# Kernel tuning notes

Hardware: AMD Instinct MI355X
Metric: run time of the kernel (lower is better)

## Reference

```python
import jax, jax.numpy as jnp
import numpy as np
from math import sqrt

B, T, I, H, O, R = 128, 1000, 3, 512, 1, 2
NOISE_STD = 0.05
ALPHA = 0.2


def setup_inputs() -> dict:
    key = jax.random.key(0)
    ks = jax.random.split(key, 6)
    inp = jax.random.normal(ks[0], (B, T, I), dtype=jnp.float32)
    noise = jax.random.normal(ks[1], (B, T, H), dtype=jnp.float32)
    # parameters initialized as in the torch module
    wi = jax.random.normal(ks[2], (I, H), dtype=jnp.float32)
    si = jnp.ones((I,), dtype=jnp.float32)
    m = jax.random.normal(ks[3], (H, R), dtype=jnp.float32) * (1.0 / sqrt(H))
    n = jax.random.normal(ks[4], (H, R), dtype=jnp.float32) * (1.0 / sqrt(H))
    wo = jax.random.normal(ks[5], (H, O), dtype=jnp.float32) * (2.0 / H)
    so = jnp.ones((O,), dtype=jnp.float32)
    h0 = jnp.zeros((H,), dtype=jnp.float32)
    return {"input": inp, "noise": noise, "wi": wi, "si": si, "m": m,
            "n": n, "wo": wo, "so": so, "h0": h0}


def reference(input, noise, wi, si, m, n, wo, so, h0):
    # proxy parameters: wi_full = (wi.T * si).T, wo_full = wo * so
    wi_full = si[:, None] * wi          # (I, H)
    wo_full = wo * so                   # (H, O)
    batch = input.shape[0]
    h_init = jnp.broadcast_to(h0, (batch, h0.shape[0]))  # (B, H)

    def step(h, xs):
        x_t, z_t = xs                   # (B, I), (B, H)
        r = jnp.tanh(h)
        rec = (r @ n) @ m.T             # low-rank recurrence, (B, H)
        h_new = h + NOISE_STD * z_t + ALPHA * (-h + rec + x_t @ wi_full)
        out = jnp.tanh(h_new) @ wo_full  # (B, O)
        return h_new, (out, h_new)

    xs = (jnp.swapaxes(input, 0, 1), jnp.swapaxes(noise, 0, 1))  # time-major
    _, (outs, hs) = jax.lax.scan(step, h_init, xs)
    output = jnp.swapaxes(outs, 0, 1)               # (B, T, O)
    trajectories = jnp.concatenate(
        [h_init[:, None, :], jnp.swapaxes(hs, 0, 1)], axis=1)  # (B, T+1, H)
    return output, trajectories
```

## Files before the change

kernel.cpp:

```cpp
#include <hip/hip_runtime.h>
#include <stdint.h>

#define B_ 128
#define T_ 1000
#define H_ 512
#define PH 8
#define NPHASE 125

typedef float vfloat4 __attribute__((ext_vector_type(4)));
typedef float vfloat2 __attribute__((ext_vector_type(2)));

template <int CTRL>
__device__ __forceinline__ float dpp_add(float x) {
    int moved = __builtin_amdgcn_update_dpp(0, __float_as_int(x), CTRL, 0xf, 0xf, true);
    return x + __int_as_float(moved);
}

__device__ __forceinline__ void wave_reduce2(float& p0, float& p1) {
    p0 = dpp_add<0x111>(p0); p1 = dpp_add<0x111>(p1);
    p0 = dpp_add<0x112>(p0); p1 = dpp_add<0x112>(p1);
    p0 = dpp_add<0x114>(p0); p1 = dpp_add<0x114>(p1);
    p0 = dpp_add<0x118>(p0); p1 = dpp_add<0x118>(p1);
    p0 = dpp_add<0x142>(p0); p1 = dpp_add<0x142>(p1);
    p0 = dpp_add<0x143>(p0); p1 = dpp_add<0x143>(p1);
}

__device__ __forceinline__ float wave_reduce1(float p) {
    p = dpp_add<0x111>(p); p = dpp_add<0x112>(p); p = dpp_add<0x114>(p);
    p = dpp_add<0x118>(p); p = dpp_add<0x142>(p); p = dpp_add<0x143>(p);
    return p;
}

__device__ __forceinline__ float fast_tanh(float x) {
    float E = __builtin_amdgcn_exp2f(x * 2.885390081777927f);
    float r = __builtin_amdgcn_rcpf(E + 1.0f);
    return __builtin_fmaf(-2.0f, r, 1.0f);
}

#define C2_ 2.885390081777927f

__device__ __forceinline__ vfloat2 bc2(float x) { vfloat2 v = {x, x}; return v; }

__global__ __launch_bounds__(128, 1) void lowrank_rnn_kernel(
    const float* __restrict__ input,
    const float* __restrict__ noise,
    const float* __restrict__ wi,
    const float* __restrict__ si,
    const float* __restrict__ m,
    const float* __restrict__ n,
    const float* __restrict__ wo,
    const float* __restrict__ so,
    const float* __restrict__ h0,
    float* __restrict__ out)
{
    const int b    = blockIdx.x;
    const int tid  = threadIdx.x;
    const int wid  = tid >> 6;
    const int lane = tid & 63;
    const int j0   = lane * 8;

    __shared__ __align__(16) vfloat4 ub[2][PH][2][64];
    __shared__ __align__(16) vfloat4 rb[2][PH][2][64];
    __shared__ __align__(16) vfloat4 hb[2][PH][2][64];
    __shared__ __align__(16) vfloat4 rfin[2][64];
    __shared__ __align__(16) vfloat4 hfin[2][64];
    __shared__ float os[T_ + 1];
    __shared__ int   flags[2];

    if (tid == 0) { flags[0] = 0; flags[1] = 0; }
    __syncthreads();
    volatile int* vprod = &flags[0];
    volatile int* vcons = &flags[1];

    if (wid == 1) {
        float wS0[8], wS1[8], wS2[8], wof[8];
        {
            const float so0 = so[0];
            #pragma unroll
            for (int i = 0; i < 3; ++i) {
                float s = 0.2f * si[i];
                float* dst = (i == 0) ? wS0 : (i == 1) ? wS1 : wS2;
                #pragma unroll
                for (int q = 0; q < 2; ++q) {
                    vfloat4 vw = *(const vfloat4*)(wi + i * H_ + j0 + 4 * q);
                    dst[4*q] = vw.x * s; dst[4*q+1] = vw.y * s;
                    dst[4*q+2] = vw.z * s; dst[4*q+3] = vw.w * s;
                }
            }
            #pragma unroll
            for (int q = 0; q < 2; ++q) {
                vfloat4 vw = *(const vfloat4*)(wo + j0 + 4 * q);
                wof[4*q] = vw.x * so0; wof[4*q+1] = vw.y * so0;
                wof[4*q+2] = vw.z * so0; wof[4*q+3] = vw.w * so0;
            }
        }
        const float* zb = noise + (size_t)b * T_ * H_ + j0;
        const float* xb = input + (size_t)b * T_ * 3;
        float* trajBase = out + (size_t)B_ * T_ + (size_t)b * (T_ + 1) * H_;

        {
            vfloat4 a = *(const vfloat4*)(h0 + j0);
            vfloat4 c = *(const vfloat4*)(h0 + j0 + 4);
            *(vfloat4*)(trajBase + j0)     = a;
            *(vfloat4*)(trajBase + j0 + 4) = c;
        }

        auto emit_phase = [&](int pp) {
            const int hf = pp & 1;
            #pragma unroll
            for (int s = 0; s < PH; ++s) {
                const int t = pp * PH + s;
                vfloat4 rl = rb[hf][s][0][lane];
                vfloat4 rh = rb[hf][s][1][lane];
                float p2 = rl.x * wof[0];
                p2 = __builtin_fmaf(rl.y, wof[1], p2);
                p2 = __builtin_fmaf(rl.z, wof[2], p2);
                p2 = __builtin_fmaf(rl.w, wof[3], p2);
                p2 = __builtin_fmaf(rh.x, wof[4], p2);
                p2 = __builtin_fmaf(rh.y, wof[5], p2);
                p2 = __builtin_fmaf(rh.z, wof[6], p2);
                p2 = __builtin_fmaf(rh.w, wof[7], p2);
                p2 = wave_reduce1(p2);
                if (lane == 63) os[t] = p2;
                vfloat4 hl = hb[hf][s][0][lane];
                vfloat4 hh = hb[hf][s][1][lane];
                float* tr = trajBase + (size_t)t * H_ + j0;
                *(vfloat4*)tr       = hl;
                *(vfloat4*)(tr + 4) = hh;
            }
        };

        for (int q = 0; q < NPHASE; ++q) {
            if (q >= 2) {
                while (*vcons < q - 1) {}
                asm volatile("" ::: "memory");
            }
            vfloat4 zl[PH], zh[PH];
            #pragma unroll
            for (int s = 0; s < PH; ++s) {
                const float* g = zb + (size_t)(q * PH + s) * H_;
                zl[s] = *(const vfloat4*)g;
                zh[s] = *(const vfloat4*)(g + 4);
            }
            if (q >= 2) emit_phase(q - 2);
            const int half = q & 1;
            #pragma unroll
            for (int s = 0; s < PH; ++s) {
                const int t = q * PH + s;
                float x0 = xb[3*t], x1 = xb[3*t+1], x2 = xb[3*t+2];
                float zz[8] = {zl[s].x, zl[s].y, zl[s].z, zl[s].w,
                               zh[s].x, zh[s].y, zh[s].z, zh[s].w};
                float u[8];
                #pragma unroll
                for (int k = 0; k < 8; ++k) {
                    float xw = __builtin_fmaf(x0, wS0[k],
                               __builtin_fmaf(x1, wS1[k], x2 * wS2[k]));
                    u[k] = __builtin_fmaf(zz[k], 0.05f, xw);
                }
                vfloat4 ulo = {u[0], u[1], u[2], u[3]};
                vfloat4 uhi = {u[4], u[5], u[6], u[7]};
                ub[half][s][0][lane] = ulo;
                ub[half][s][1][lane] = uhi;
            }
            asm volatile("s_waitcnt lgkmcnt(0)" ::: "memory");
            if (lane == 0) *vprod = q + 1;
        }
        while (*vcons < NPHASE) {}
        asm volatile("" ::: "memory");
        emit_phase(NPHASE - 2);
        emit_phase(NPHASE - 1);
        while (*vcons < NPHASE + 1) {}
        asm volatile("" ::: "memory");
        {
            vfloat4 rl = rfin[0][lane], rh = rfin[1][lane];
            float p2 = rl.x * wof[0];
            p2 = __builtin_fmaf(rl.y, wof[1], p2);
            p2 = __builtin_fmaf(rl.z, wof[2], p2);
            p2 = __builtin_fmaf(rl.w, wof[3], p2);
            p2 = __builtin_fmaf(rh.x, wof[4], p2);
            p2 = __builtin_fmaf(rh.y, wof[5], p2);
            p2 = __builtin_fmaf(rh.z, wof[6], p2);
            p2 = __builtin_fmaf(rh.w, wof[7], p2);
            p2 = wave_reduce1(p2);
            if (lane == 63) os[T_] = p2;
            float* tr = trajBase + (size_t)T_ * H_ + j0;
            *(vfloat4*)tr       = hfin[0][lane];
            *(vfloat4*)(tr + 4) = hfin[1][lane];
        }
        asm volatile("s_waitcnt lgkmcnt(0)" ::: "memory");
        float* outp = out + (size_t)b * T_;
        for (int idx = lane; idx < T_; idx += 64)
            outp[idx] = os[idx + 1];
    } else {
        vfloat2 n02[4], n12[4], m02[4], m12[4];
        vfloat2 bP[2][4], Tc[2][4], Dc[2][4];
        {
            const float* nb = n + 2 * j0;
            const float* mb = m + 2 * j0;
            #pragma unroll
            for (int q = 0; q < 4; ++q) {
                vfloat4 vn = *(const vfloat4*)(nb + 4 * q);
                vfloat2 a = {vn.x, vn.z}; n02[q] = a;
                vfloat2 c = {vn.y, vn.w}; n12[q] = c;
                vfloat4 vm = *(const vfloat4*)(mb + 4 * q);
                vfloat2 d = {0.2f * vm.x, 0.2f * vm.z}; m02[q] = d;
                vfloat2 e = {0.2f * vm.y, 0.2f * vm.w}; m12[q] = e;
            }
            #pragma unroll
            for (int q = 0; q < 2; ++q) {
                vfloat4 vh = *(const vfloat4*)(h0 + j0 + 4 * q);
                vfloat2 lo = {vh.x, vh.y}, hi = {vh.z, vh.w};
                bP[0][2*q] = lo; bP[0][2*q+1] = hi;
            }
            #pragma unroll
            for (int j = 0; j < 4; ++j) {
                vfloat2 T = {fast_tanh(bP[0][j].x), fast_tanh(bP[0][j].y)};
                Tc[0][j] = T;
                Dc[0][j] = 1.0f - T * T;
            }
        }
        float a0s = 0.0f, a1s = 0.0f;

        for (int p = 0; p < NPHASE; ++p) {
            while (*vprod < p + 1) {}
            asm volatile("" ::: "memory");
            const int half = p & 1;
            vfloat4 cul = ub[half][0][0][lane];
            vfloat4 cuh = ub[half][0][1][lane];
            #pragma unroll
            for (int s = 0; s < PH; ++s) {
                const int pp = s & 1;
                const int np = pp ^ 1;
                vfloat4 nul, nuh;
                if (s < PH - 1) {
                    nul = ub[half][s+1][0][lane];
                    nuh = ub[half][s+1][1][lane];
                }
                vfloat2 a02 = bc2(a0s), a12 = bc2(a1s);

                vfloat2 dl[4], r2[4], h2[4];
                #pragma unroll
                for (int j = 0; j < 4; ++j)
                    dl[j] = a02 * m02[j] + a12 * m12[j];
                #pragma unroll
                for (int j = 0; j < 4; ++j) {
                    vfloat2 t1 = Tc[pp][j] * dl[j];
                    vfloat2 e  = dl[j] - t1 * dl[j];
                    r2[j] = Dc[pp][j] * e + Tc[pp][j];
                }
                vfloat2 A0 = r2[1] * n02[1] + r2[0] * n02[0];
                vfloat2 B0 = r2[3] * n02[3] + r2[2] * n02[2];
                vfloat2 P0 = A0 + B0;
                float p0 = P0.x + P0.y;
                vfloat2 A1 = r2[1] * n12[1] + r2[0] * n12[0];
                vfloat2 B1 = r2[3] * n12[3] + r2[2] * n12[2];
                vfloat2 P1 = A1 + B1;
                float p1 = P1.x + P1.y;
                wave_reduce2(p0, p1);

                vfloat2 u2[4];
                vfloat2 t0 = {cul.x, cul.y}; u2[0] = t0;
                vfloat2 t1v = {cul.z, cul.w}; u2[1] = t1v;
                vfloat2 t2 = {cuh.x, cuh.y}; u2[2] = t2;
                vfloat2 t3 = {cuh.z, cuh.w}; u2[3] = t3;
                #pragma unroll
                for (int j = 0; j < 4; ++j) {
                    h2[j] = bP[pp][j] + dl[j];
                    bP[np][j] = h2[j] * 0.8f + u2[j];
                }
                #pragma unroll
                for (int j = 0; j < 4; ++j) {
                    vfloat2 x2 = bP[np][j] * C2_;
                    vfloat2 E  = {__builtin_amdgcn_exp2f(x2.x),
                                  __builtin_amdgcn_exp2f(x2.y)};
                    vfloat2 DD = E + 1.0f;
                    vfloat2 R  = {__builtin_amdgcn_rcpf(DD.x),
                                  __builtin_amdgcn_rcpf(DD.y)};
                    vfloat2 T  = bc2(-2.0f) * R + 1.0f;
                    Tc[np][j] = T;
                    Dc[np][j] = 1.0f - T * T;
                }

                vfloat4 rlo = {r2[0].x, r2[0].y, r2[1].x, r2[1].y};
                vfloat4 rhi = {r2[2].x, r2[2].y, r2[3].x, r2[3].y};
                rb[half][s][0][lane] = rlo;
                rb[half][s][1][lane] = rhi;
                vfloat4 hlo = {h2[0].x, h2[0].y, h2[1].x, h2[1].y};
                vfloat4 hhi = {h2[2].x, h2[2].y, h2[3].x, h2[3].y};
                hb[half][s][0][lane] = hlo;
                hb[half][s][1][lane] = hhi;

                a0s = __int_as_float(__builtin_amdgcn_readlane(__float_as_int(p0), 63));
                a1s = __int_as_float(__builtin_amdgcn_readlane(__float_as_int(p1), 63));

                cul = nul; cuh = nuh;
            }
            asm volatile("s_waitcnt lgkmcnt(0)" ::: "memory");
            if (lane == 0) *vcons = p + 1;
        }
        while (*vprod < NPHASE) {}
        asm volatile("" ::: "memory");
        vfloat2 a02 = bc2(a0s), a12 = bc2(a1s);
        float r[8], hT8[8];
        #pragma unroll
        for (int j = 0; j < 4; ++j) {
            vfloat2 dlt = a02 * m02[j] + a12 * m12[j];
            vfloat2 hT  = bP[0][j] + dlt;
            hT8[2*j] = hT.x; hT8[2*j+1] = hT.y;
            r[2*j]   = fast_tanh(hT.x);
            r[2*j+1] = fast_tanh(hT.y);
        }
        vfloat4 rlo = {r[0], r[1], r[2], r[3]};
        vfloat4 rhi = {r[4], r[5], r[6], r[7]};
        rfin[0][lane] = rlo;
        rfin[1][lane] = rhi;
        vfloat4 hlo = {hT8[0], hT8[1], hT8[2], hT8[3]};
        vfloat4 hhi = {hT8[4], hT8[5], hT8[6], hT8[7]};
        hfin[0][lane] = hlo;
        hfin[1][lane] = hhi;
        asm volatile("s_waitcnt lgkmcnt(0)" ::: "memory");
        if (lane == 0) *vcons = NPHASE + 1;
    }
}

extern "C" void kernel_launch(void* const* d_in, const int* in_sizes, int n_in,
                              void* d_out, int out_size, void* d_ws, size_t ws_size,
                              hipStream_t stream) {
    const float* input = (const float*)d_in[0];
    const float* noise = (const float*)d_in[1];
    const float* wi    = (const float*)d_in[2];
    const float* si    = (const float*)d_in[3];
    const float* m     = (const float*)d_in[4];
    const float* n     = (const float*)d_in[5];
    const float* wo    = (const float*)d_in[6];
    const float* so    = (const float*)d_in[7];
    const float* h0    = (const float*)d_in[8];
    float* out = (float*)d_out;

    hipLaunchKernelGGL(lowrank_rnn_kernel, dim3(B_), dim3(128), 0, stream,
                       input, noise, wi, si, m, n, wo, so, h0, out);
}
```

Before: 294.5 us.

## Double phase length and recompute tanh in producer wave instead of LDS r buffer

Raises the steps per synchronisation phase from 8 to 16, so there are half as many producer/consumer flag handshakes, and adds a tail phase of 8 steps for the remainder. The recurrence wave no longer writes tanh(h) to LDS. The helper wave recomputes tanh from the stored h when forming the output projection, which takes LDS stores off the critical serial path. In exchange the helper wave does extra transcendental work per step, and noise loads are split into two half-phase batches to limit register pressure.

```diff
diff --git a/kernel.cpp b/kernel.cpp
--- a/kernel.cpp
+++ b/kernel.cpp
@@ -4,8 +4,8 @@
 #define B_ 128
 #define T_ 1000
 #define H_ 512
-#define PH 8
-#define NPHASE 125
+#define PH 16
+#define NFULL 62
 
 typedef float vfloat4 __attribute__((ext_vector_type(4)));
 typedef float vfloat2 __attribute__((ext_vector_type(2)));
@@ -60,9 +60,7 @@
     const int j0   = lane * 8;
 
     __shared__ __align__(16) vfloat4 ub[2][PH][2][64];
-    __shared__ __align__(16) vfloat4 rb[2][PH][2][64];
     __shared__ __align__(16) vfloat4 hb[2][PH][2][64];
-    __shared__ __align__(16) vfloat4 rfin[2][64];
     __shared__ __align__(16) vfloat4 hfin[2][64];
     __shared__ float os[T_ + 1];
     __shared__ int   flags[2];
@@ -105,51 +103,41 @@
             *(vfloat4*)(trajBase + j0 + 4) = c;
         }
 
-        auto emit_phase = [&](int pp) {
+        auto emit_half = [&](int pp, int hh) {
             const int hf = pp & 1;
             #pragma unroll
-            for (int s = 0; s < PH; ++s) {
+            for (int s8 = 0; s8 < 8; ++s8) {
+                const int s = hh * 8 + s8;
                 const int t = pp * PH + s;
-                vfloat4 rl = rb[hf][s][0][lane];
-                vfloat4 rh = rb[hf][s][1][lane];
-                float p2 = rl.x * wof[0];
-                p2 = __builtin_fmaf(rl.y, wof[1], p2);
-                p2 = __builtin_fmaf(rl.z, wof[2], p2);
-                p2 = __builtin_fmaf(rl.w, wof[3], p2);
-                p2 = __builtin_fmaf(rh.x, wof[4], p2);
-                p2 = __builtin_fmaf(rh.y, wof[5], p2);
-                p2 = __builtin_fmaf(rh.z, wof[6], p2);
-                p2 = __builtin_fmaf(rh.w, wof[7], p2);
+                vfloat4 hl = hb[hf][s][0][lane];
+                vfloat4 hh4 = hb[hf][s][1][lane];
+                float r0 = fast_tanh(hl.x), r1 = fast_tanh(hl.y);
+                float r2 = fast_tanh(hl.z), r3 = fast_tanh(hl.w);
+                float r4 = fast_tanh(hh4.x), r5 = fast_tanh(hh4.y);
+                float r6 = fast_tanh(hh4.z), r7 = fast_tanh(hh4.w);
+                float p2 = r0 * wof[0];
+                p2 = __builtin_fmaf(r1, wof[1], p2);
+                p2 = __builtin_fmaf(r2, wof[2], p2);
+                p2 = __builtin_fmaf(r3, wof[3], p2);
+                p2 = __builtin_fmaf(r4, wof[4], p2);
+                p2 = __builtin_fmaf(r5, wof[5], p2);
+                p2 = __builtin_fmaf(r6, wof[6], p2);
+                p2 = __builtin_fmaf(r7, wof[7], p2);
                 p2 = wave_reduce1(p2);
                 if (lane == 63) os[t] = p2;
-                vfloat4 hl = hb[hf][s][0][lane];
-                vfloat4 hh = hb[hf][s][1][lane];
                 float* tr = trajBase + (size_t)t * H_ + j0;
                 *(vfloat4*)tr       = hl;
-                *(vfloat4*)(tr + 4) = hh;
+                *(vfloat4*)(tr + 4) = hh4;
             }
         };
 
-        for (int q = 0; q < NPHASE; ++q) {
-            if (q >= 2) {
-                while (*vcons < q - 1) {}
-                asm volatile("" ::: "memory");
-            }
-            vfloat4 zl[PH], zh[PH];
-            #pragma unroll
-            for (int s = 0; s < PH; ++s) {
-                const float* g = zb + (size_t)(q * PH + s) * H_;
-                zl[s] = *(const vfloat4*)g;
-                zh[s] = *(const vfloat4*)(g + 4);
-            }
-            if (q >= 2) emit_phase(q - 2);
-            const int half = q & 1;
-            #pragma unroll
-            for (int s = 0; s < PH; ++s) {
-                const int t = q * PH + s;
+        auto make_u8 = [&](int t0, int half, int s0, vfloat4* zl, vfloat4* zh) {
+            #pragma unroll
+            for (int k8 = 0; k8 < 8; ++k8) {
+                const int t = t0 + k8;
                 float x0 = xb[3*t], x1 = xb[3*t+1], x2 = xb[3*t+2];
-                float zz[8] = {zl[s].x, zl[s].y, zl[s].z, zl[s].w,
-                               zh[s].x, zh[s].y, zh[s].z, zh[s].w};
+                float zz[8] = {zl[k8].x, zl[k8].y, zl[k8].z, zl[k8].w,
+                               zh[k8].x, zh[k8].y, zh[k8].z, zh[k8].w};
                 float u[8];
                 #pragma unroll
                 for (int k = 0; k < 8; ++k) {
@@ -159,38 +147,80 @@
                 }
                 vfloat4 ulo = {u[0], u[1], u[2], u[3]};
                 vfloat4 uhi = {u[4], u[5], u[6], u[7]};
-                ub[half][s][0][lane] = ulo;
-                ub[half][s][1][lane] = uhi;
-            }
+                ub[half][s0 + k8][0][lane] = ulo;
+                ub[half][s0 + k8][1][lane] = uhi;
+            }
+        };
+
+        for (int q = 0; q < NFULL; ++q) {
+            if (q >= 2) {
+                while (*vcons < q - 1) {}
+                asm volatile("" ::: "memory");
+            }
+            const int half = q & 1;
+            vfloat4 zl[8], zh[8];
+            #pragma unroll
+            for (int s = 0; s < 8; ++s) {
+                const float* g = zb + (size_t)(q * PH + s) * H_;
+                zl[s] = *(const vfloat4*)g;
+                zh[s] = *(const vfloat4*)(g + 4);
+            }
+            if (q >= 2) emit_half(q - 2, 0);
+            make_u8(q * PH, half, 0, zl, zh);
+            #pragma unroll
+            for (int s = 0; s < 8; ++s) {
+                const float* g = zb + (size_t)(q * PH + 8 + s) * H_;
+                zl[s] = *(const vfloat4*)g;
+                zh[s] = *(const vfloat4*)(g + 4);
+            }
+            if (q >= 2) emit_half(q - 2, 1);
+            make_u8(q * PH + 8, half, 8, zl, zh);
             asm volatile("s_waitcnt lgkmcnt(0)" ::: "memory");
             if (lane == 0) *vprod = q + 1;
         }
-        while (*vcons < NPHASE) {}
-        asm volatile("" ::: "memory");
-        emit_phase(NPHASE - 2);
-        emit_phase(NPHASE - 1);
-        while (*vcons < NPHASE + 1) {}
-        asm volatile("" ::: "memory");
-        {
-            vfloat4 rl = rfin[0][lane], rh = rfin[1][lane];
-            float p2 = rl.x * wof[0];
-            p2 = __builtin_fmaf(rl.y, wof[1], p2);
-            p2 = __builtin_fmaf(rl.z, wof[2], p2);
-            p2 = __builtin_fmaf(rl.w, wof[3], p2);
-            p2 = __builtin_fmaf(rh.x, wof[4], p2);
-            p2 = __builtin_fmaf(rh.y, wof[5], p2);
-            p2 = __builtin_fmaf(rh.z, wof[6], p2);
-            p2 = __builtin_fmaf(rh.w, wof[7], p2);
-            p2 = wave_reduce1(p2);
-            if (lane == 63) os[T_] = p2;
-            float* tr = trajBase + (size_t)T_ * H_ + j0;
-            *(vfloat4*)tr       = hfin[0][lane];
-            *(vfloat4*)(tr + 4) = hfin[1][lane];
-        }
-        asm volatile("s_waitcnt lgkmcnt(0)" ::: "memory");
-        float* outp = out + (size_t)b * T_;
-        for (int idx = lane; idx < T_; idx += 64)
-            outp[idx] = os[idx + 1];
+        {
+            while (*vcons < NFULL - 1) {}
+            asm volatile("" ::: "memory");
+            vfloat4 zl[8], zh[8];
+            #pragma unroll
+            for (int s = 0; s < 8; ++s) {
+                const float* g = zb + (size_t)(NFULL * PH + s) * H_;
+                zl[s] = *(const vfloat4*)g;
+                zh[s] = *(const vfloat4*)(g + 4);
+            }
+            emit_half(NFULL - 2, 0); emit_half(NFULL - 2, 1);
+            make_u8(NFULL * PH, 0, 0, zl, zh);
+            asm volatile("s_waitcnt lgkmcnt(0)" ::: "memory");
+            if (lane == 0) *vprod = NFULL + 1;
+            while (*vcons < NFULL) {}
+            asm volatile("" ::: "memory");
+            emit_half(NFULL - 1, 0); emit_half(NFULL - 1, 1);
+            while (*vcons < NFULL + 1) {}
+            asm volatile("" ::: "memory");
+            emit_half(NFULL, 0);
+            while (*vcons < NFULL + 2) {}
+            asm volatile("" ::: "memory");
+            {
+                vfloat4 hl = hfin[0][lane], hh4 = hfin[1][lane];
+                float p2 = fast_tanh(hl.x) * wof[0];
+                p2 = __builtin_fmaf(fast_tanh(hl.y), wof[1], p2);
+                p2 = __builtin_fmaf(fast_tanh(hl.z), wof[2], p2);
+                p2 = __builtin_fmaf(fast_tanh(hl.w), wof[3], p2);
+                p2 = __builtin_fmaf(fast_tanh(hh4.x), wof[4], p2);
+                p2 = __builtin_fmaf(fast_tanh(hh4.y), wof[5], p2);
+                p2 = __builtin_fmaf(fast_tanh(hh4.z), wof[6], p2);
+                p2 = __builtin_fmaf(fast_tanh(hh4.w), wof[7], p2);
+                p2 = wave_reduce1(p2);
+                if (lane == 63) os[T_] = p2;
+                float* tr = trajBase + (size_t)T_ * H_ + j0;
+                *(vfloat4*)tr       = hl;
+                *(vfloat4*)(tr + 4) = hh4;
+            }
+            asm volatile("s_waitcnt lgkmcnt(0)" ::: "memory");
+            float* outp = out + (size_t)b * T_;
+            for (int idx = lane; idx < T_; idx += 64)
+                outp[idx] = os[idx + 1];
+        }
     } else {
         vfloat2 n02[4], n12[4], m02[4], m12[4];
         vfloat2 bP[2][4], Tc[2][4], Dc[2][4];
@@ -221,105 +251,98 @@
         }
         float a0s = 0.0f, a1s = 0.0f;
 
-        for (int p = 0; p < NPHASE; ++p) {
+        auto STEP = [&](int half, int s, int L) {
+            const int pp = s & 1;
+            const int np = pp ^ 1;
+            vfloat4 cul = ub[half][s][0][lane];
+            vfloat4 cuh = ub[half][s][1][lane];
+            vfloat2 a02 = bc2(a0s), a12 = bc2(a1s);
+
+            vfloat2 dl[4], r2[4], h2[4];
+            #pragma unroll
+            for (int j = 0; j < 4; ++j)
+                dl[j] = a02 * m02[j] + a12 * m12[j];
+            #pragma unroll
+            for (int j = 0; j < 4; ++j) {
+                vfloat2 t1 = Tc[pp][j] * dl[j];
+                vfloat2 e  = dl[j] - t1 * dl[j];
+                r2[j] = Dc[pp][j] * e + Tc[pp][j];
+            }
+            vfloat2 A0 = r2[1] * n02[1] + r2[0] * n02[0];
+            vfloat2 B0 = r2[3] * n02[3] + r2[2] * n02[2];
+            vfloat2 P0 = A0 + B0;
+            float p0 = P0.x + P0.y;
+            vfloat2 A1 = r2[1] * n12[1] + r2[0] * n12[0];
+            vfloat2 B1 = r2[3] * n12[3] + r2[2] * n12[2];
+            vfloat2 P1 = A1 + B1;
+            float p1 = P1.x + P1.y;
+            wave_reduce2(p0, p1);
+
+            vfloat2 u2[4];
+            vfloat2 t0 = {cul.x, cul.y}; u2[0] = t0;
+            vfloat2 t1v = {cul.z, cul.w}; u2[1] = t1v;
+            vfloat2 t2 = {cuh.x, cuh.y}; u2[2] = t2;
+            vfloat2 t3 = {cuh.z, cuh.w}; u2[3] = t3;
+            #pragma unroll
+            for (int j = 0; j < 4; ++j) {
+                h2[j] = bP[pp][j] + dl[j];
+                bP[np][j] = h2[j] * 0.8f + u2[j];
+            }
+            #pragma unroll
+            for (int j = 0; j < 4; ++j) {
+                vfloat2 x2 = bP[np][j] * C2_;
+                vfloat2 E  = {__builtin_amdgcn_exp2f(x2.x),
+                              __builtin_amdgcn_exp2f(x2.y)};
+                vfloat2 DD = E + 1.0f;
+                vfloat2 R  = {__builtin_amdgcn_rcpf(DD.x),
+                              __builtin_amdgcn_rcpf(DD.y)};
+                vfloat2 T  = bc2(-2.0f) * R + 1.0f;
+                Tc[np][j] = T;
+                Dc[np][j] = 1.0f - T * T;
+            }
+
+            vfloat4 hlo = {h2[0].x, h2[0].y, h2[1].x, h2[1].y};
+            vfloat4 hhi = {h2[2].x, h2[2].y, h2[3].x, h2[3].y};
+            hb[half][s][0][lane] = hlo;
+            hb[half][s][1][lane] = hhi;
+
+            a0s = __int_as_float(__builtin_amdgcn_readlane(__float_as_int(p0), 63));
+            a1s = __int_as_float(__builtin_amdgcn_readlane(__float_as_int(p1), 63));
+        };
+
+        for (int p = 0; p < NFULL; ++p) {
             while (*vprod < p + 1) {}
             asm volatile("" ::: "memory");
             const int half = p & 1;
-            vfloat4 cul = ub[half][0][0][lane];
-            vfloat4 cuh = ub[half][0][1][lane];
-            #pragma unroll
-            for (int s = 0; s < PH; ++s) {
-                const int pp = s & 1;
-                const int np = pp ^ 1;
-                vfloat4 nul, nuh;
-                if (s < PH - 1) {
-                    nul = ub[half][s+1][0][lane];
-                    nuh = ub[half][s+1][1][lane];
-                }
-                vfloat2 a02 = bc2(a0s), a12 = bc2(a1s);
-
-                vfloat2 dl[4], r2[4], h2[4];
-                #pragma unroll
-                for (int j = 0; j < 4; ++j)
-                    dl[j] = a02 * m02[j] + a12 * m12[j];
-                #pragma unroll
-                for (int j = 0; j < 4; ++j) {
-                    vfloat2 t1 = Tc[pp][j] * dl[j];
-                    vfloat2 e  = dl[j] - t1 * dl[j];
-                    r2[j] = Dc[pp][j] * e + Tc[pp][j];
-                }
-                vfloat2 A0 = r2[1] * n02[1] + r2[0] * n02[0];
-                vfloat2 B0 = r2[3] * n02[3] + r2[2] * n02[2];
-                vfloat2 P0 = A0 + B0;
-                float p0 = P0.x + P0.y;
-                vfloat2 A1 = r2[1] * n12[1] + r2[0] * n12[0];
-                vfloat2 B1 = r2[3] * n12[3] + r2[2] * n12[2];
-                vfloat2 P1 = A1 + B1;
-                float p1 = P1.x + P1.y;
-                wave_reduce2(p0, p1);
-
-                vfloat2 u2[4];
-                vfloat2 t0 = {cul.x, cul.y}; u2[0] = t0;
-                vfloat2 t1v = {cul.z, cul.w}; u2[1] = t1v;
-                vfloat2 t2 = {cuh.x, cuh.y}; u2[2] = t2;
-                vfloat2 t3 = {cuh.z, cuh.w}; u2[3] = t3;
-                #pragma unroll
-                for (int j = 0; j < 4; ++j) {
-                    h2[j] = bP[pp][j] + dl[j];
-                    bP[np][j] = h2[j] * 0.8f + u2[j];
-                }
-                #pragma unroll
-                for (int j = 0; j < 4; ++j) {
-                    vfloat2 x2 = bP[np][j] * C2_;
-                    vfloat2 E  = {__builtin_amdgcn_exp2f(x2.x),
-                                  __builtin_amdgcn_exp2f(x2.y)};
-                    vfloat2 DD = E + 1.0f;
-                    vfloat2 R  = {__builtin_amdgcn_rcpf(DD.x),
-                                  __builtin_amdgcn_rcpf(DD.y)};
-                    vfloat2 T  = bc2(-2.0f) * R + 1.0f;
-                    Tc[np][j] = T;
-                    Dc[np][j] = 1.0f - T * T;
-                }
-
-                vfloat4 rlo = {r2[0].x, r2[0].y, r2[1].x, r2[1].y};
-                vfloat4 rhi = {r2[2].x, r2[2].y, r2[3].x, r2[3].y};
-                rb[half][s][0][lane] = rlo;
-                rb[half][s][1][lane] = rhi;
-                vfloat4 hlo = {h2[0].x, h2[0].y, h2[1].x, h2[1].y};
-                vfloat4 hhi = {h2[2].x, h2[2].y, h2[3].x, h2[3].y};
-                hb[half][s][0][lane] = hlo;
-                hb[half][s][1][lane] = hhi;
-
-                a0s = __int_as_float(__builtin_amdgcn_readlane(__float_as_int(p0), 63));
-                a1s = __int_as_float(__builtin_amdgcn_readlane(__float_as_int(p1), 63));
-
-                cul = nul; cuh = nuh;
-            }
+            #pragma unroll
+            for (int s = 0; s < PH; ++s) STEP(half, s, PH);
             asm volatile("s_waitcnt lgkmcnt(0)" ::: "memory");
             if (lane == 0) *vcons = p + 1;
         }
-        while (*vprod < NPHASE) {}
-        asm volatile("" ::: "memory");
-        vfloat2 a02 = bc2(a0s), a12 = bc2(a1s);
-        float r[8], hT8[8];
-        #pragma unroll
-        for (int j = 0; j < 4; ++j) {
-            vfloat2 dlt = a02 * m02[j] + a12 * m12[j];
-            vfloat2 hT  = bP[0][j] + dlt;
-            hT8[2*j] = hT.x; hT8[2*j+1] = hT.y;
-            r[2*j]   = fast_tanh(hT.x);
-            r[2*j+1] = fast_tanh(hT.y);
-        }
-        vfloat4 rlo = {r[0], r[1], r[2], r[3]};
-        vfloat4 rhi = {r[4], r[5], r[6], r[7]};
-        rfin[0][lane] = rlo;
-        rfin[1][lane] = rhi;
-        vfloat4 hlo = {hT8[0], hT8[1], hT8[2], hT8[3]};
-        vfloat4 hhi = {hT8[4], hT8[5], hT8[6], hT8[7]};
-        hfin[0][lane] = hlo;
-        hfin[1][lane] = hhi;
-        asm volatile("s_waitcnt lgkmcnt(0)" ::: "memory");
-        if (lane == 0) *vcons = NPHASE + 1;
+        {
+            while (*vprod < NFULL + 1) {}
+            asm volatile("" ::: "memory");
+            #pragma unroll
+            for (int s = 0; s < 8; ++s) STEP(0, s, 8);
+            asm volatile("s_waitcnt lgkmcnt(0)" ::: "memory");
+            if (lane == 0) *vcons = NFULL + 1;
+        }
+        {
+            vfloat2 a02 = bc2(a0s), a12 = bc2(a1s);
+            float hT8[8];
+            #pragma unroll
+            for (int j = 0; j < 4; ++j) {
+                vfloat2 dlt = a02 * m02[j] + a12 * m12[j];
+                vfloat2 hT  = bP[0][j] + dlt;
+                hT8[2*j] = hT.x; hT8[2*j+1] = hT.y;
+            }
+            vfloat4 hlo = {hT8[0], hT8[1], hT8[2], hT8[3]};
+            vfloat4 hhi = {hT8[4], hT8[5], hT8[6], hT8[7]};
+            hfin[0][lane] = hlo;
+            hfin[1][lane] = hhi;
+            asm volatile("s_waitcnt lgkmcnt(0)" ::: "memory");
+            if (lane == 0) *vcons = NFULL + 2;
+        }
     }
 }
 
```

Result: slower. 350.4 us (+19.0%).
